# Optimization experiments

Measured on AMD Instinct MI355X. Metric: run time of the kernel, lower is better.

Reference implementation:

```python
import jax, jax.numpy as jnp
import numpy as np

W_DIM = 512
LRELU_SLOPE = 0.2
ACT_GAIN = np.sqrt(2.0).astype(np.float32)  # def_gain for lrelu, gain=1


def setup_inputs() -> dict:
    key = jax.random.key(0)
    k1, k2, k3, k4 = jax.random.split(key, 4)
    B, Cin, Cout, R, K = 8, 128, 128, 32, 3
    return {
        "x": jax.random.normal(k1, (B, Cin, R, R, R), dtype=jnp.float32),
        "w": jax.random.normal(k2, (B, W_DIM), dtype=jnp.float32),
        "weight": jax.random.normal(k3, (Cout, Cin, K, K, K), dtype=jnp.float32),
        "affine_weight": jax.random.normal(k4, (Cin, W_DIM), dtype=jnp.float32),
        "affine_bias": jnp.ones((Cin,), dtype=jnp.float32),
        "bias": jnp.zeros((Cout,), dtype=jnp.float32),
    }


def _conv_one(xi, wi):
    # xi: [Cin, D, H, W], wi: [Cout, Cin, k, k, k] -> [Cout, D, H, W]
    return jax.lax.conv_general_dilated(
        xi[None], wi, window_strides=(1, 1, 1),
        padding=[(1, 1), (1, 1), (1, 1)],
        dimension_numbers=("NCDHW", "OIDHW", "NCDHW"))[0]


def reference(x, w, weight, affine_weight, affine_bias, bias):
    B = x.shape[0]
    # affine: FullyConnectedLayer, linear, weight_gain = 1/sqrt(w_dim), bias_gain=1
    styles = w @ (affine_weight * (1.0 / np.sqrt(W_DIM))).T + affine_bias  # [B, Cin]
    # modulate
    wmod = weight[None] * styles[:, None, :, None, None, None]  # [B, Cout, Cin, k, k, k]
    # demodulate
    dcoefs = jax.lax.rsqrt(jnp.sum(jnp.square(wmod), axis=(2, 3, 4, 5)) + 1e-8)  # [B, Cout]
    wmod = wmod * dcoefs[:, :, None, None, None, None]
    # grouped conv (groups = batch) == vmap of per-sample conv
    out = jax.vmap(_conv_one)(x, wmod)  # [B, Cout, R, R, R]
    # bias_act: lrelu with gain=sqrt(2), clamp=None (noise path is disabled in forward)
    out = out + bias[None, :, None, None, None]
    out = jnp.where(out >= 0, out, out * LRELU_SLOPE) * ACT_GAIN
    return out
```

## Files before the change

kernel.cpp:

```cpp
#include <hip/hip_runtime.h>
#include <hip/hip_bf16.h>

typedef __attribute__((ext_vector_type(8))) short bf16x8;
typedef __attribute__((ext_vector_type(4))) float f32x4;

#define WDIM 512
#define CIN 128
#define COUT 128
#define NRES 32
#define NSP 32768
#define NTAPS 27

#define ROWB 2112
#define LDSROWS 16
#define BUFB (LDSROWS * ROWB)

#define ZP_OFF 4096
#define XT_OFF 8192
#define WM_OFF (8192 + 67108864)

typedef __attribute__((address_space(1))) const unsigned int gu32;
typedef __attribute__((address_space(3))) unsigned int lu32;

__global__ void k_styles(const float* __restrict__ w,
                         const float* __restrict__ aw,
                         const float* __restrict__ ab,
                         float* __restrict__ styles,
                         float* __restrict__ zeropad) {
  int b = blockIdx.x;
  int c = threadIdx.x;
  if (b == 0) {
#pragma unroll
    for (int i = 0; i < 8; i++) zeropad[i * 128 + c] = 0.f;
  }
  const float4* wr = (const float4*)(w + (size_t)b * WDIM);
  const float4* ar = (const float4*)(aw + (size_t)c * WDIM);
  float s = 0.f;
#pragma unroll 8
  for (int k = 0; k < WDIM / 4; k++) {
    float4 wv = wr[k], av = ar[k];
    s += wv.x * av.x + wv.y * av.y + wv.z * av.z + wv.w * av.w;
  }
  styles[b * CIN + c] = s * 0.04419417382415922f + ab[c];
}

__global__ void k_wmod(const float* __restrict__ weight,
                       const float* __restrict__ styles,
                       __hip_bfloat16* __restrict__ wmod) {
  int b = blockIdx.x >> 7;
  int co = blockIdx.x & 127;
  __shared__ float st[CIN];
  __shared__ float red[4];
  int tid = threadIdx.x;
  if (tid < CIN) st[tid] = styles[b * CIN + tid];
  __syncthreads();
  const float* wr = weight + (size_t)co * (CIN * NTAPS);
  float ss = 0.f;
  for (int o = tid; o < CIN * NTAPS; o += 256) {
    float v = wr[o] * st[o / NTAPS];
    ss += v * v;
  }
#pragma unroll
  for (int off = 32; off > 0; off >>= 1) ss += __shfl_down(ss, off);
  if ((tid & 63) == 0) red[tid >> 6] = ss;
  __syncthreads();
  float d = rsqrtf(red[0] + red[1] + red[2] + red[3] + 1e-8f);
  for (int o = tid; o < CIN * NTAPS; o += 256) {
    int t = o >> 7;
    int cin = o & 127;
    float v = wr[cin * NTAPS + t] * st[cin] * d;
    int cc = cin >> 5, cl = cin & 31;
    wmod[((((size_t)(b * 4 + cc) * COUT + co) * NTAPS + t) << 5) + cl] =
        __float2bfloat16(v);
  }
}

__global__ __launch_bounds__(256)
void k_xt(const float* __restrict__ x, __hip_bfloat16* __restrict__ xt) {
  __shared__ __align__(16) float ts[32][257];
  int t = threadIdx.x;
  int blk = blockIdx.x;
  int b = blk >> 9, cc = (blk >> 7) & 3, sp0 = (blk & 127) << 8;
  const float* xb = x + (size_t)b * CIN * NSP + (size_t)cc * 32 * NSP + sp0;
#pragma unroll
  for (int i = 0; i < 8; i++) {
    int q = i * 256 + t;
    int cin = q >> 6, f4 = q & 63;
    float4 v = *(const float4*)(xb + (size_t)cin * NSP + f4 * 4);
    *(float4*)&ts[cin][f4 * 4] = v;
  }
  __syncthreads();
  __hip_bfloat16* ob = xt + ((size_t)(b * 4 + cc) * NSP + sp0) * 32;
#pragma unroll
  for (int j = 0; j < 4; j++) {
    int chunk = j * 256 + t;
    int sp_l = chunk >> 2, q = chunk & 3;
    union { bf16x8 v; __hip_bfloat16 h[8]; } u;
#pragma unroll
    for (int k = 0; k < 8; k++) u.h[k] = __float2bfloat16(ts[q * 8 + k][sp_l]);
    *(bf16x8*)(ob + (size_t)sp_l * 32 + q * 8) = u.v;
  }
}

__global__ __launch_bounds__(256, 2)
void k_conv(const char* __restrict__ ws,
            const float* __restrict__ bias,
            float* __restrict__ out) {
  extern __shared__ __align__(16) char xs[];

  int tid = threadIdx.x;
  int lane = tid & 63, w = tid >> 6;
  int l15 = lane & 15, g = lane >> 4;
  int blk = blockIdx.x;
  int b = blk & 7;
  int tile = blk >> 3;
  int z0 = (tile >> 4) * 2, y0 = (tile & 15) * 2;

  {
    int r16 = tid >> 4, c16 = (tid & 15) * 4;
    *(int*)&xs[r16 * ROWB + 2048 + c16] = 0;
    *(int*)&xs[BUFB + r16 * ROWB + 2048 + c16] = 0;
  }

  int soff[8], sdst[8], svalid[8];
#pragma unroll
  for (int i = 0; i < 8; i++) {
    int c = i * 256 + tid;
    int zy = c >> 7;
    int hz = zy >> 2, hy = zy & 3;
    int zz = z0 + hz - 1, yy = y0 + hy - 1;
    svalid[i] = ((unsigned)zz < NRES) & ((unsigned)yy < NRES);
    int p = c & 127, hx = p >> 2, pos = p & 3;
    int q = pos ^ ((hx >> 1) & 3);
    soff[i] = (zz * 1024 + yy * 32 + hx) * 4 + q;
    sdst[i] = zy * ROWB + (p >> 6) * 1024;
  }

  int vaddr[8][3];
#pragma unroll
  for (int ni = 0; ni < 8; ni++) {
    int row = (ni >> 2) * 4 + ((ni >> 1) & 1);
    int dx = (ni & 1) * 16 + l15;
#pragma unroll
    for (int tx = 0; tx < 3; tx++) {
      int hx = dx + tx - 1;
      int hxc = ((unsigned)hx > 31u) ? 32 : hx;
      int pos = g ^ ((hxc >> 1) & 3);
      vaddr[ni][tx] = row * ROWB + hxc * 64 + pos * 16;
    }
  }

  const bf16x8* ap = (const bf16x8*)(ws + WM_OFF);
  int abase[2];
#pragma unroll
  for (int mi = 0; mi < 2; mi++)
    abase[mi] = (w * 32 + mi * 16 + l15) * 108 + g;

  f32x4 acc[2][8];
#pragma unroll
  for (int mi = 0; mi < 2; mi++)
#pragma unroll
    for (int ni = 0; ni < 8; ni++) acc[mi][ni] = (f32x4){0.f, 0.f, 0.f, 0.f};

  const char* zpg = ws + ZP_OFF;
  const char* xtb = ws + XT_OFF + (size_t)b * (4 * NSP * 64);

  auto stage = [&](char* dst, const char* xtc) {
#pragma unroll
    for (int i = 0; i < 8; i++) {
      const char* src = svalid[i] ? (xtc + ((size_t)(unsigned)soff[i] << 4))
                                  : (zpg + lane * 16);
      __builtin_amdgcn_global_load_lds((gu32*)src, (lu32*)(dst + sdst[i]), 16, 0, 0);
    }
  };

  stage(xs, xtb);
  __syncthreads();

#pragma unroll 1
  for (int cc = 0; cc < 4; cc++) {
    char* cur = xs + (cc & 1) * BUFB;
    int sab = ((b * 4 + cc) * 128) * 108;
    int abc0 = sab + abase[0], abc1 = sab + abase[1];

    bf16x8 A[2][2], B[2][8];
    A[0][0] = ap[abc0]; A[0][1] = ap[abc1];
#pragma unroll
    for (int j = 0; j < 8; j++) B[0][j] = *(const bf16x8*)(cur + vaddr[j][0]);

#pragma unroll
    for (int t = 0; t < NTAPS; t++) {
      const int s = t & 1, ns = s ^ 1;
      const int t1 = t + 1;
      if (t < NTAPS - 1) {
        A[ns][0] = ap[abc0 + t1 * 4];
        A[ns][1] = ap[abc1 + t1 * 4];
      }
      if (t == 1 && cc < 3) {
        __builtin_amdgcn_sched_barrier(0);
        stage(xs + ((cc + 1) & 1) * BUFB, xtb + (size_t)(cc + 1) * (NSP * 64));
        __builtin_amdgcn_sched_barrier(0);
      }
      if (t < NTAPS - 1) {
        const int tx1 = t1 % 3;
        const int lit1 = ((t1 / 9) * 4 + (t1 / 3) % 3) * ROWB;
#pragma unroll
        for (int j = 0; j < 8; j++)
          B[ns][j] = *(const bf16x8*)(cur + vaddr[j][tx1] + lit1);
      }
      __builtin_amdgcn_s_setprio(1);
#pragma unroll
      for (int mi = 0; mi < 2; mi++) {
        acc[mi][0] = __builtin_amdgcn_mfma_f32_16x16x32_bf16(A[s][mi], B[s][0], acc[mi][0], 0, 0, 0);
        acc[mi][1] = __builtin_amdgcn_mfma_f32_16x16x32_bf16(A[s][mi], B[s][1], acc[mi][1], 0, 0, 0);
        acc[mi][2] = __builtin_amdgcn_mfma_f32_16x16x32_bf16(A[s][mi], B[s][2], acc[mi][2], 0, 0, 0);
        acc[mi][3] = __builtin_amdgcn_mfma_f32_16x16x32_bf16(A[s][mi], B[s][3], acc[mi][3], 0, 0, 0);
        acc[mi][4] = __builtin_amdgcn_mfma_f32_16x16x32_bf16(A[s][mi], B[s][4], acc[mi][4], 0, 0, 0);
        acc[mi][5] = __builtin_amdgcn_mfma_f32_16x16x32_bf16(A[s][mi], B[s][5], acc[mi][5], 0, 0, 0);
        acc[mi][6] = __builtin_amdgcn_mfma_f32_16x16x32_bf16(A[s][mi], B[s][6], acc[mi][6], 0, 0, 0);
        acc[mi][7] = __builtin_amdgcn_mfma_f32_16x16x32_bf16(A[s][mi], B[s][7], acc[mi][7], 0, 0, 0);
      }
      __builtin_amdgcn_s_setprio(0);
    }
    if (cc < 3) __syncthreads();
  }

  size_t ob = ((size_t)(b * COUT + w * 32 + g * 4)) * NSP +
              (size_t)z0 * 1024 + (size_t)y0 * 32;
#pragma unroll
  for (int mi = 0; mi < 2; mi++) {
    float4 bsv = *(const float4*)(bias + w * 32 + mi * 16 + g * 4);
    float bs[4] = {bsv.x, bsv.y, bsv.z, bsv.w};
#pragma unroll
    for (int ni = 0; ni < 8; ni++) {
      int spo = (ni >> 2) * 1024 + ((ni >> 1) & 1) * 32 + (ni & 1) * 16 + l15;
#pragma unroll
      for (int r = 0; r < 4; r++) {
        float v = acc[mi][ni][r] + bs[r];
        v = (v >= 0.f ? v : v * 0.2f) * 1.41421356237309515f;
        out[ob + (size_t)(mi * 16 + r) * NSP + spo] = v;
      }
    }
  }
}

extern "C" void kernel_launch(void* const* d_in, const int* in_sizes, int n_in,
                              void* d_out, int out_size, void* d_ws, size_t ws_size,
                              hipStream_t stream) {
  const float* x      = (const float*)d_in[0];
  const float* w      = (const float*)d_in[1];
  const float* weight = (const float*)d_in[2];
  const float* aw     = (const float*)d_in[3];
  const float* ab     = (const float*)d_in[4];
  const float* bias   = (const float*)d_in[5];
  float* out = (float*)d_out;

  float* styles = (float*)d_ws;
  float* zeropad = (float*)((char*)d_ws + ZP_OFF);
  __hip_bfloat16* xt = (__hip_bfloat16*)((char*)d_ws + XT_OFF);
  __hip_bfloat16* wmod = (__hip_bfloat16*)((char*)d_ws + WM_OFF);

  k_styles<<<8, 128, 0, stream>>>(w, aw, ab, styles, zeropad);
  k_wmod<<<8 * 128, 256, 0, stream>>>(weight, styles, wmod);
  k_xt<<<8 * 4 * 128, 256, 0, stream>>>(x, xt);
  k_conv<<<8 * 256, 256, 2 * BUFB, stream>>>((const char*)d_ws, bias, out);
}
```

Before: 240.2 us.

## Fuse style computation into wmod kernel and retile conv warps to 64x64

The separate styles kernel is folded into the wmod kernel. Each block now recomputes the style dot products for its batch, split across two thread halves, which removes one launch and the dependency gap between kernels but repeats the affine work 128 times per batch. In the conv kernel, each wave now covers 64 output channels by 64 spatial positions (4x4 MFMA tiles) instead of 32x128. This cuts LDS B-fragment reads per MFMA in exchange for more global A-fragment loads.

```diff
diff --git a/kernel.cpp b/kernel.cpp
--- a/kernel.cpp
+++ b/kernel.cpp
@@ -22,37 +22,38 @@
 typedef __attribute__((address_space(1))) const unsigned int gu32;
 typedef __attribute__((address_space(3))) unsigned int lu32;
 
-__global__ void k_styles(const float* __restrict__ w,
-                         const float* __restrict__ aw,
-                         const float* __restrict__ ab,
-                         float* __restrict__ styles,
-                         float* __restrict__ zeropad) {
-  int b = blockIdx.x;
-  int c = threadIdx.x;
-  if (b == 0) {
-#pragma unroll
-    for (int i = 0; i < 8; i++) zeropad[i * 128 + c] = 0.f;
-  }
-  const float4* wr = (const float4*)(w + (size_t)b * WDIM);
-  const float4* ar = (const float4*)(aw + (size_t)c * WDIM);
-  float s = 0.f;
-#pragma unroll 8
-  for (int k = 0; k < WDIM / 4; k++) {
-    float4 wv = wr[k], av = ar[k];
-    s += wv.x * av.x + wv.y * av.y + wv.z * av.z + wv.w * av.w;
-  }
-  styles[b * CIN + c] = s * 0.04419417382415922f + ab[c];
-}
-
-__global__ void k_wmod(const float* __restrict__ weight,
-                       const float* __restrict__ styles,
-                       __hip_bfloat16* __restrict__ wmod) {
+__global__ __launch_bounds__(256)
+void k_wmod(const float* __restrict__ w,
+            const float* __restrict__ aw,
+            const float* __restrict__ ab,
+            const float* __restrict__ weight,
+            float* __restrict__ zeropad,
+            __hip_bfloat16* __restrict__ wmod) {
   int b = blockIdx.x >> 7;
   int co = blockIdx.x & 127;
+  int tid = threadIdx.x;
+  if (blockIdx.x == 0) {
+#pragma unroll
+    for (int i = 0; i < 4; i++) zeropad[i * 256 + tid] = 0.f;
+  }
+  __shared__ float stp[256];
   __shared__ float st[CIN];
   __shared__ float red[4];
-  int tid = threadIdx.x;
-  if (tid < CIN) st[tid] = styles[b * CIN + tid];
+  {
+    int c = tid & 127, half = tid >> 7;
+    const float4* wr = (const float4*)(w + (size_t)b * WDIM + half * 256);
+    const float4* ar = (const float4*)(aw + (size_t)c * WDIM + half * 256);
+    float s = 0.f;
+#pragma unroll 8
+    for (int k = 0; k < 64; k++) {
+      float4 wv = wr[k], av = ar[k];
+      s += wv.x * av.x + wv.y * av.y + wv.z * av.z + wv.w * av.w;
+    }
+    stp[tid] = s;
+  }
+  __syncthreads();
+  if (tid < 128)
+    st[tid] = (stp[tid] + stp[tid + 128]) * 0.04419417382415922f + ab[tid];
   __syncthreads();
   const float* wr = weight + (size_t)co * (CIN * NTAPS);
   float ss = 0.f;
@@ -111,6 +112,7 @@
   int tid = threadIdx.x;
   int lane = tid & 63, w = tid >> 6;
   int l15 = lane & 15, g = lane >> 4;
+  int w2 = w >> 1, wz = w & 1;
   int blk = blockIdx.x;
   int b = blk & 7;
   int tile = blk >> 3;
@@ -136,10 +138,10 @@
     sdst[i] = zy * ROWB + (p >> 6) * 1024;
   }
 
-  int vaddr[8][3];
-#pragma unroll
-  for (int ni = 0; ni < 8; ni++) {
-    int row = (ni >> 2) * 4 + ((ni >> 1) & 1);
+  int vaddr[4][3];
+#pragma unroll
+  for (int ni = 0; ni < 4; ni++) {
+    int row = wz * 4 + (ni >> 1);
     int dx = (ni & 1) * 16 + l15;
 #pragma unroll
     for (int tx = 0; tx < 3; tx++) {
@@ -151,16 +153,16 @@
   }
 
   const bf16x8* ap = (const bf16x8*)(ws + WM_OFF);
-  int abase[2];
-#pragma unroll
-  for (int mi = 0; mi < 2; mi++)
-    abase[mi] = (w * 32 + mi * 16 + l15) * 108 + g;
-
-  f32x4 acc[2][8];
-#pragma unroll
-  for (int mi = 0; mi < 2; mi++)
-#pragma unroll
-    for (int ni = 0; ni < 8; ni++) acc[mi][ni] = (f32x4){0.f, 0.f, 0.f, 0.f};
+  int abase[4];
+#pragma unroll
+  for (int mi = 0; mi < 4; mi++)
+    abase[mi] = (w2 * 64 + mi * 16 + l15) * 108 + g;
+
+  f32x4 acc[4][4];
+#pragma unroll
+  for (int mi = 0; mi < 4; mi++)
+#pragma unroll
+    for (int ni = 0; ni < 4; ni++) acc[mi][ni] = (f32x4){0.f, 0.f, 0.f, 0.f};
 
   const char* zpg = ws + ZP_OFF;
   const char* xtb = ws + XT_OFF + (size_t)b * (4 * NSP * 64);
@@ -181,20 +183,23 @@
   for (int cc = 0; cc < 4; cc++) {
     char* cur = xs + (cc & 1) * BUFB;
     int sab = ((b * 4 + cc) * 128) * 108;
-    int abc0 = sab + abase[0], abc1 = sab + abase[1];
-
-    bf16x8 A[2][2], B[2][8];
-    A[0][0] = ap[abc0]; A[0][1] = ap[abc1];
-#pragma unroll
-    for (int j = 0; j < 8; j++) B[0][j] = *(const bf16x8*)(cur + vaddr[j][0]);
+    int abc[4];
+#pragma unroll
+    for (int mi = 0; mi < 4; mi++) abc[mi] = sab + abase[mi];
+
+    bf16x8 A[2][4], B[2][4];
+#pragma unroll
+    for (int mi = 0; mi < 4; mi++) A[0][mi] = ap[abc[mi]];
+#pragma unroll
+    for (int j = 0; j < 4; j++) B[0][j] = *(const bf16x8*)(cur + vaddr[j][0]);
 
 #pragma unroll
     for (int t = 0; t < NTAPS; t++) {
       const int s = t & 1, ns = s ^ 1;
       const int t1 = t + 1;
       if (t < NTAPS - 1) {
-        A[ns][0] = ap[abc0 + t1 * 4];
-        A[ns][1] = ap[abc1 + t1 * 4];
+#pragma unroll
+        for (int mi = 0; mi < 4; mi++) A[ns][mi] = ap[abc[mi] + t1 * 4];
       }
       if (t == 1 && cc < 3) {
         __builtin_amdgcn_sched_barrier(0);
@@ -205,35 +210,31 @@
         const int tx1 = t1 % 3;
         const int lit1 = ((t1 / 9) * 4 + (t1 / 3) % 3) * ROWB;
 #pragma unroll
-        for (int j = 0; j < 8; j++)
+        for (int j = 0; j < 4; j++)
           B[ns][j] = *(const bf16x8*)(cur + vaddr[j][tx1] + lit1);
       }
       __builtin_amdgcn_s_setprio(1);
 #pragma unroll
-      for (int mi = 0; mi < 2; mi++) {
+      for (int mi = 0; mi < 4; mi++) {
         acc[mi][0] = __builtin_amdgcn_mfma_f32_16x16x32_bf16(A[s][mi], B[s][0], acc[mi][0], 0, 0, 0);
         acc[mi][1] = __builtin_amdgcn_mfma_f32_16x16x32_bf16(A[s][mi], B[s][1], acc[mi][1], 0, 0, 0);
         acc[mi][2] = __builtin_amdgcn_mfma_f32_16x16x32_bf16(A[s][mi], B[s][2], acc[mi][2], 0, 0, 0);
         acc[mi][3] = __builtin_amdgcn_mfma_f32_16x16x32_bf16(A[s][mi], B[s][3], acc[mi][3], 0, 0, 0);
-        acc[mi][4] = __builtin_amdgcn_mfma_f32_16x16x32_bf16(A[s][mi], B[s][4], acc[mi][4], 0, 0, 0);
-        acc[mi][5] = __builtin_amdgcn_mfma_f32_16x16x32_bf16(A[s][mi], B[s][5], acc[mi][5], 0, 0, 0);
-        acc[mi][6] = __builtin_amdgcn_mfma_f32_16x16x32_bf16(A[s][mi], B[s][6], acc[mi][6], 0, 0, 0);
-        acc[mi][7] = __builtin_amdgcn_mfma_f32_16x16x32_bf16(A[s][mi], B[s][7], acc[mi][7], 0, 0, 0);
       }
       __builtin_amdgcn_s_setprio(0);
     }
     if (cc < 3) __syncthreads();
   }
 
-  size_t ob = ((size_t)(b * COUT + w * 32 + g * 4)) * NSP +
-              (size_t)z0 * 1024 + (size_t)y0 * 32;
-#pragma unroll
-  for (int mi = 0; mi < 2; mi++) {
-    float4 bsv = *(const float4*)(bias + w * 32 + mi * 16 + g * 4);
+  size_t ob = ((size_t)(b * COUT + w2 * 64 + g * 4)) * NSP +
+              (size_t)(z0 + wz) * 1024 + (size_t)y0 * 32;
+#pragma unroll
+  for (int mi = 0; mi < 4; mi++) {
+    float4 bsv = *(const float4*)(bias + w2 * 64 + mi * 16 + g * 4);
     float bs[4] = {bsv.x, bsv.y, bsv.z, bsv.w};
 #pragma unroll
-    for (int ni = 0; ni < 8; ni++) {
-      int spo = (ni >> 2) * 1024 + ((ni >> 1) & 1) * 32 + (ni & 1) * 16 + l15;
+    for (int ni = 0; ni < 4; ni++) {
+      int spo = (ni >> 1) * 32 + (ni & 1) * 16 + l15;
 #pragma unroll
       for (int r = 0; r < 4; r++) {
         float v = acc[mi][ni][r] + bs[r];
@@ -255,13 +256,11 @@
   const float* bias   = (const float*)d_in[5];
   float* out = (float*)d_out;
 
-  float* styles = (float*)d_ws;
   float* zeropad = (float*)((char*)d_ws + ZP_OFF);
   __hip_bfloat16* xt = (__hip_bfloat16*)((char*)d_ws + XT_OFF);
   __hip_bfloat16* wmod = (__hip_bfloat16*)((char*)d_ws + WM_OFF);
 
-  k_styles<<<8, 128, 0, stream>>>(w, aw, ab, styles, zeropad);
-  k_wmod<<<8 * 128, 256, 0, stream>>>(weight, styles, wmod);
+  k_wmod<<<8 * 128, 256, 0, stream>>>(w, aw, ab, weight, zeropad, wmod);
   k_xt<<<8 * 4 * 128, 256, 0, stream>>>(x, xt);
   k_conv<<<8 * 256, 256, 2 * BUFB, stream>>>((const char*)d_ws, bias, out);
 }
```

New measurement: 321.7 us. 1.34x slower.

## Fuse style affine into wmod kernel and deepen conv A-operand prefetch

Applied to the files above, without the earlier changes.

Removes the separate styles kernel: each wmod block recomputes its batch's 128 styles with a two-half split dot product over w_dim, saving one launch and a dependent global round trip at the cost of redundant affine work across the 128 blocks per batch. In the conv kernel, the next-chunk LDS staging is issued before the tap loop instead of at tap 1. The global A-operand (modulated weight) prefetch is deepened from double buffering to a 4-deep register ring refilled after each tap's MFMAs, to hide global load latency. This raises VGPR pressure, which may reduce occupancy.

```diff
diff --git a/kernel.cpp b/kernel.cpp
--- a/kernel.cpp
+++ b/kernel.cpp
@@ -22,37 +22,38 @@
 typedef __attribute__((address_space(1))) const unsigned int gu32;
 typedef __attribute__((address_space(3))) unsigned int lu32;
 
-__global__ void k_styles(const float* __restrict__ w,
-                         const float* __restrict__ aw,
-                         const float* __restrict__ ab,
-                         float* __restrict__ styles,
-                         float* __restrict__ zeropad) {
-  int b = blockIdx.x;
-  int c = threadIdx.x;
-  if (b == 0) {
-#pragma unroll
-    for (int i = 0; i < 8; i++) zeropad[i * 128 + c] = 0.f;
-  }
-  const float4* wr = (const float4*)(w + (size_t)b * WDIM);
-  const float4* ar = (const float4*)(aw + (size_t)c * WDIM);
-  float s = 0.f;
-#pragma unroll 8
-  for (int k = 0; k < WDIM / 4; k++) {
-    float4 wv = wr[k], av = ar[k];
-    s += wv.x * av.x + wv.y * av.y + wv.z * av.z + wv.w * av.w;
-  }
-  styles[b * CIN + c] = s * 0.04419417382415922f + ab[c];
-}
-
-__global__ void k_wmod(const float* __restrict__ weight,
-                       const float* __restrict__ styles,
-                       __hip_bfloat16* __restrict__ wmod) {
+__global__ __launch_bounds__(256)
+void k_wmod(const float* __restrict__ w,
+            const float* __restrict__ aw,
+            const float* __restrict__ ab,
+            const float* __restrict__ weight,
+            float* __restrict__ zeropad,
+            __hip_bfloat16* __restrict__ wmod) {
   int b = blockIdx.x >> 7;
   int co = blockIdx.x & 127;
+  int tid = threadIdx.x;
+  if (blockIdx.x == 0) {
+#pragma unroll
+    for (int i = 0; i < 4; i++) zeropad[i * 256 + tid] = 0.f;
+  }
+  __shared__ float stp[256];
   __shared__ float st[CIN];
   __shared__ float red[4];
-  int tid = threadIdx.x;
-  if (tid < CIN) st[tid] = styles[b * CIN + tid];
+  {
+    int c = tid & 127, half = tid >> 7;
+    const float4* wr = (const float4*)(w + (size_t)b * WDIM + half * 256);
+    const float4* ar = (const float4*)(aw + (size_t)c * WDIM + half * 256);
+    float s = 0.f;
+#pragma unroll 8
+    for (int k = 0; k < 64; k++) {
+      float4 wv = wr[k], av = ar[k];
+      s += wv.x * av.x + wv.y * av.y + wv.z * av.z + wv.w * av.w;
+    }
+    stp[tid] = s;
+  }
+  __syncthreads();
+  if (tid < 128)
+    st[tid] = (stp[tid] + stp[tid + 128]) * 0.04419417382415922f + ab[tid];
   __syncthreads();
   const float* wr = weight + (size_t)co * (CIN * NTAPS);
   float ss = 0.f;
@@ -183,44 +184,48 @@
     int sab = ((b * 4 + cc) * 128) * 108;
     int abc0 = sab + abase[0], abc1 = sab + abase[1];
 
-    bf16x8 A[2][2], B[2][8];
-    A[0][0] = ap[abc0]; A[0][1] = ap[abc1];
+    bf16x8 A[4][2], B[2][8];
+#pragma unroll
+    for (int pt = 0; pt < 4; pt++) {
+      A[pt][0] = ap[abc0 + pt * 4];
+      A[pt][1] = ap[abc1 + pt * 4];
+    }
 #pragma unroll
     for (int j = 0; j < 8; j++) B[0][j] = *(const bf16x8*)(cur + vaddr[j][0]);
+    __builtin_amdgcn_sched_barrier(0);
+    if (cc < 3)
+      stage(xs + ((cc + 1) & 1) * BUFB, xtb + (size_t)(cc + 1) * (NSP * 64));
+    __builtin_amdgcn_sched_barrier(0);
 
 #pragma unroll
     for (int t = 0; t < NTAPS; t++) {
-      const int s = t & 1, ns = s ^ 1;
-      const int t1 = t + 1;
+      const int s = t & 3;
+      const int sb = t & 1, nsb = sb ^ 1;
       if (t < NTAPS - 1) {
-        A[ns][0] = ap[abc0 + t1 * 4];
-        A[ns][1] = ap[abc1 + t1 * 4];
-      }
-      if (t == 1 && cc < 3) {
-        __builtin_amdgcn_sched_barrier(0);
-        stage(xs + ((cc + 1) & 1) * BUFB, xtb + (size_t)(cc + 1) * (NSP * 64));
-        __builtin_amdgcn_sched_barrier(0);
-      }
-      if (t < NTAPS - 1) {
+        const int t1 = t + 1;
         const int tx1 = t1 % 3;
         const int lit1 = ((t1 / 9) * 4 + (t1 / 3) % 3) * ROWB;
 #pragma unroll
         for (int j = 0; j < 8; j++)
-          B[ns][j] = *(const bf16x8*)(cur + vaddr[j][tx1] + lit1);
+          B[nsb][j] = *(const bf16x8*)(cur + vaddr[j][tx1] + lit1);
       }
       __builtin_amdgcn_s_setprio(1);
 #pragma unroll
       for (int mi = 0; mi < 2; mi++) {
-        acc[mi][0] = __builtin_amdgcn_mfma_f32_16x16x32_bf16(A[s][mi], B[s][0], acc[mi][0], 0, 0, 0);
-        acc[mi][1] = __builtin_amdgcn_mfma_f32_16x16x32_bf16(A[s][mi], B[s][1], acc[mi][1], 0, 0, 0);
-        acc[mi][2] = __builtin_amdgcn_mfma_f32_16x16x32_bf16(A[s][mi], B[s][2], acc[mi][2], 0, 0, 0);
-        acc[mi][3] = __builtin_amdgcn_mfma_f32_16x16x32_bf16(A[s][mi], B[s][3], acc[mi][3], 0, 0, 0);
-        acc[mi][4] = __builtin_amdgcn_mfma_f32_16x16x32_bf16(A[s][mi], B[s][4], acc[mi][4], 0, 0, 0);
-        acc[mi][5] = __builtin_amdgcn_mfma_f32_16x16x32_bf16(A[s][mi], B[s][5], acc[mi][5], 0, 0, 0);
-        acc[mi][6] = __builtin_amdgcn_mfma_f32_16x16x32_bf16(A[s][mi], B[s][6], acc[mi][6], 0, 0, 0);
-        acc[mi][7] = __builtin_amdgcn_mfma_f32_16x16x32_bf16(A[s][mi], B[s][7], acc[mi][7], 0, 0, 0);
+        acc[mi][0] = __builtin_amdgcn_mfma_f32_16x16x32_bf16(A[s][mi], B[sb][0], acc[mi][0], 0, 0, 0);
+        acc[mi][1] = __builtin_amdgcn_mfma_f32_16x16x32_bf16(A[s][mi], B[sb][1], acc[mi][1], 0, 0, 0);
+        acc[mi][2] = __builtin_amdgcn_mfma_f32_16x16x32_bf16(A[s][mi], B[sb][2], acc[mi][2], 0, 0, 0);
+        acc[mi][3] = __builtin_amdgcn_mfma_f32_16x16x32_bf16(A[s][mi], B[sb][3], acc[mi][3], 0, 0, 0);
+        acc[mi][4] = __builtin_amdgcn_mfma_f32_16x16x32_bf16(A[s][mi], B[sb][4], acc[mi][4], 0, 0, 0);
+        acc[mi][5] = __builtin_amdgcn_mfma_f32_16x16x32_bf16(A[s][mi], B[sb][5], acc[mi][5], 0, 0, 0);
+        acc[mi][6] = __builtin_amdgcn_mfma_f32_16x16x32_bf16(A[s][mi], B[sb][6], acc[mi][6], 0, 0, 0);
+        acc[mi][7] = __builtin_amdgcn_mfma_f32_16x16x32_bf16(A[s][mi], B[sb][7], acc[mi][7], 0, 0, 0);
       }
       __builtin_amdgcn_s_setprio(0);
+      if (t + 4 < NTAPS) {
+        A[s][0] = ap[abc0 + (t + 4) * 4];
+        A[s][1] = ap[abc1 + (t + 4) * 4];
+      }
     }
     if (cc < 3) __syncthreads();
   }
@@ -255,13 +260,11 @@
   const float* bias   = (const float*)d_in[5];
   float* out = (float*)d_out;
 
-  float* styles = (float*)d_ws;
   float* zeropad = (float*)((char*)d_ws + ZP_OFF);
   __hip_bfloat16* xt = (__hip_bfloat16*)((char*)d_ws + XT_OFF);
   __hip_bfloat16* wmod = (__hip_bfloat16*)((char*)d_ws + WM_OFF);
 
-  k_styles<<<8, 128, 0, stream>>>(w, aw, ab, styles, zeropad);
-  k_wmod<<<8 * 128, 256, 0, stream>>>(weight, styles, wmod);
+  k_wmod<<<8 * 128, 256, 0, stream>>>(w, aw, ab, weight, zeropad, wmod);
   k_xt<<<8 * 4 * 128, 256, 0, stream>>>(x, xt);
   k_conv<<<8 * 256, 256, 2 * BUFB, stream>>>((const char*)d_ws, bias, out);
 }
```

New measurement: 260.0 us. +8.2%, slower.
